# Performance work log

Hardware: AMD Instinct MI355X
Metric: run time of the kernel (lower is better)

The kernel has to match this reference:

```python
import jax, jax.numpy as jnp
from jax import lax
import numpy as np

NT, NGRID, NX = 365, 3000, 20
H, NY = 256, 1


def setup_inputs() -> dict:
    key = jax.random.key(0)
    ks = jax.random.split(key, 12)
    x = jax.random.normal(ks[0], (NT, NGRID, NX), dtype=jnp.float32)
    y = jax.random.normal(ks[1], (NT, NGRID, NY), dtype=jnp.float32)
    obs_mask = jax.random.bernoulli(ks[2], 0.7, (NT, NGRID, NY))
    y = jnp.where(obs_mask, y, jnp.nan)
    s_in = 1.0 / np.sqrt(NX + 1)
    s_h = 1.0 / np.sqrt(H)
    w_in = jax.random.uniform(ks[3], (H, NX + 1), jnp.float32, -s_in, s_in)
    b_in = jax.random.uniform(ks[4], (H,), jnp.float32, -s_in, s_in)
    w_ih = jax.random.uniform(ks[5], (4 * H, H), jnp.float32, -s_h, s_h)
    b_ih = jax.random.uniform(ks[6], (4 * H,), jnp.float32, -s_h, s_h)
    w_hh = jax.random.uniform(ks[7], (4 * H, H), jnp.float32, -s_h, s_h)
    b_hh = jax.random.uniform(ks[8], (4 * H,), jnp.float32, -s_h, s_h)
    w_out = jax.random.uniform(ks[9], (NY, H), jnp.float32, -s_h, s_h)
    b_out = jax.random.uniform(ks[10], (NY,), jnp.float32, -s_h, s_h)
    return {"x": x, "y": y, "w_in": w_in, "b_in": b_in, "w_ih": w_ih,
            "b_ih": b_ih, "w_hh": w_hh, "b_hh": b_hh, "w_out": w_out,
            "b_out": b_out}


def reference(x, y, w_in, b_in, w_ih, b_ih, w_hh, b_hh, w_out, b_out):
    nt, ngrid, nx = x.shape
    h0 = jnp.zeros((ngrid, H), x.dtype)
    c0 = jnp.zeros((ngrid, H), x.dtype)
    y0 = jnp.zeros((ngrid, NY), x.dtype)

    def step(carry, inp):
        h, c, yt = carry
        xt, yobs = inp                      # [ngrid,nx], [ngrid,ny]
        mask = ~jnp.isnan(yobs)
        yt = jnp.where(mask, yobs, yt)      # fill observed values
        xcat = jnp.concatenate([xt, yt], axis=1)          # [ngrid, nx+1]
        x0 = jax.nn.relu(xcat @ w_in.T + b_in)            # [ngrid, H]
        gates = x0 @ w_ih.T + b_ih + h @ w_hh.T + b_hh    # [ngrid, 4H]
        i, f, g, o = jnp.split(gates, 4, axis=1)
        c = jax.nn.sigmoid(f) * c + jax.nn.sigmoid(i) * jnp.tanh(g)
        h = jax.nn.sigmoid(o) * jnp.tanh(c)
        yt_new = h @ w_out.T + b_out                      # [ngrid, ny]
        return (h, c, yt_new), yt_new

    _, out = lax.scan(step, (h0, c0, y0), (x, y))
    return out  # [nt, ngrid, ny]
```

## Files before the change

kernel.cpp:

```cpp
#include <hip/hip_runtime.h>
#include <math.h>

#define NT     365
#define NGRID  3000
#define NX     20
#define H      256
#define CPB    15
#define NBLK   (NGRID/CPB)
#define THREADS 1024

#define WPK_US   (16*16*4*64*8)
#define WPKIN_US (16*2*64*8)

typedef short v8s __attribute__((ext_vector_type(8)));
typedef float v4f __attribute__((ext_vector_type(4)));
#define MFMA_BF16 __builtin_amdgcn_mfma_f32_16x16x32_bf16

__device__ __forceinline__ unsigned short f2bf(float f) {
    unsigned int u = __float_as_uint(f);
    u += 0x7fffu + ((u >> 16) & 1u);
    return (unsigned short)(u >> 16);
}
__device__ __forceinline__ float bf2f(unsigned short h) {
    return __uint_as_float(((unsigned int)h) << 16);
}
__device__ __forceinline__ float sigm(float x)  { return 1.0f / (1.0f + __expf(-x)); }
__device__ __forceinline__ float tanh_f(float x){ return 2.0f * sigm(2.0f * x) - 1.0f; }

__global__ void prep_kernel(const float* __restrict__ w_in,
                            const float* __restrict__ w_ih,
                            const float* __restrict__ w_hh,
                            const float* __restrict__ b_ih,
                            const float* __restrict__ b_hh,
                            unsigned short* __restrict__ wpk,
                            unsigned short* __restrict__ wpkin,
                            float* __restrict__ bsum) {
    int idx = blockIdx.x * 256 + threadIdx.x;
    if (idx < WPK_US) {
        int e    = idx & 7;
        int lane = (idx >> 3) & 63;
        int q    = (idx >> 9) & 3;
        int gk   = idx >> 11;
        int kap  = gk & 15, g = gk >> 4;
        int k = kap * 32 + ((lane >> 4) << 3) + e;
        int j = q * 256 + g * 16 + (lane & 15);
        float wv = (k < 256) ? w_ih[j * 256 + k] : w_hh[j * 256 + (k - 256)];
        wpk[idx] = f2bf(wv);
    }
    if (idx < WPKIN_US) {
        int e    = idx & 7;
        int lane = (idx >> 3) & 63;
        int d    = (idx >> 9) & 1;
        int tau  = idx >> 10;
        int k = ((lane >> 4) << 3) + e;
        int n = tau * 16 + (lane & 15);
        float wv = (k < NX + 1) ? w_in[n * (NX + 1) + k] : 0.0f;
        unsigned short hi = f2bf(wv);
        wpkin[idx] = d ? f2bf(wv - bf2f(hi)) : hi;
    }
    if (idx < 4 * H) bsum[idx] = b_ih[idx] + b_hh[idx];
}

__global__ __attribute__((amdgpu_flat_work_group_size(THREADS, THREADS),
                          amdgpu_waves_per_eu(4, 4)))
void lstm_main(const float* __restrict__ x,
               const float* __restrict__ y,
               const float* __restrict__ b_in,
               const float* __restrict__ w_out,
               const float* __restrict__ b_out,
               const unsigned short* __restrict__ wpk,
               const unsigned short* __restrict__ wpkin,
               const float* __restrict__ bsum,
               float* __restrict__ out) {
    __shared__ __align__(16) unsigned short Agh[16][512];
    __shared__ __align__(16) unsigned short Agl[16][512];
    __shared__ __align__(16) unsigned short Xh[512];
    __shared__ __align__(16) unsigned short Xl[512];
    __shared__ __align__(16) unsigned short Bw11[16][2048];
    __shared__ float y_part[16][16];

    const int tid  = threadIdx.x;
    const int w    = tid >> 6;
    const int lane = tid & 63;
    const int col  = lane & 15;
    const int quad = lane >> 4;
    const int g0   = blockIdx.x * CPB;

    const int   jh   = w * 16 + col;
    const float b_i  = bsum[jh];
    const float b_f  = bsum[256 + jh];
    const float b_g  = bsum[512 + jh];
    const float b_o  = bsum[768 + jh];
    const float wo   = w_out[jh];
    const float bi_x = b_in[jh];
    const float bout = b_out[0];
    const int   kq_x = jh >> 5;
    const int   kq_h = 8 + (jh >> 5);
    const int   qp_w = (jh >> 3) & 3;
    const int   e_w  = jh & 7;
    const unsigned short* bbase = wpk + (size_t)(w * 16) * 4 * 512 + lane * 8;
    const unsigned short* bx_hi = wpkin + (w * 2 + 0) * 512 + lane * 8;
    const unsigned short* bx_lo = wpkin + (w * 2 + 1) * 512 + lane * 8;

    {
        unsigned int* p;
        p = (unsigned int*)&Agh[0][0];
        for (int i = tid; i < 16 * 256; i += THREADS) p[i] = 0u;
        p = (unsigned int*)&Agl[0][0];
        for (int i = tid; i < 16 * 256; i += THREADS) p[i] = 0u;
        if (tid < 256) ((unsigned int*)&Xh[0])[tid] = 0u;
        if (tid < 256) ((unsigned int*)&Xl[0])[tid] = 0u;
    }

#define LOADK(kap, c) (*(const v8s*)(bbase + ((size_t)(kap) * 4 + (c)) * 512))
    v8s B8_0  = LOADK(8, 0),  B8_1  = LOADK(8, 1),
        B8_2  = LOADK(8, 2),  B8_3  = LOADK(8, 3);
    v8s B9_0  = LOADK(9, 0),  B9_1  = LOADK(9, 1),
        B9_2  = LOADK(9, 2),  B9_3  = LOADK(9, 3);
    v8s B10_0 = LOADK(10, 0), B10_1 = LOADK(10, 1),
        B10_2 = LOADK(10, 2), B10_3 = LOADK(10, 3);

    {
        *(v8s*)&Bw11[w][0 * 512 + lane * 8] = LOADK(11, 0);
        *(v8s*)&Bw11[w][1 * 512 + lane * 8] = LOADK(11, 1);
        *(v8s*)&Bw11[w][2 * 512 + lane * 8] = LOADK(11, 2);
        *(v8s*)&Bw11[w][3 * 512 + lane * 8] = LOADK(11, 3);
    }

    const v8s bxh = *(const v8s*)bx_hi;
    const v8s bxl = *(const v8s*)bx_lo;

    float xv = 0.0f, yv = 0.0f;
    if (tid < CPB * NX) xv = x[(size_t)g0 * NX + tid];
    if (tid < CPB)      yv = y[(size_t)g0 + tid];

    float c_st[4];
    #pragma unroll
    for (int r = 0; r < 4; ++r) c_st[r] = 0.0f;
    __syncthreads();

#define GEMM_KAP(KAP, B0, B1, B2, B3)                                   \
    {                                                                   \
        v8s Ah = *(const v8s*)&Agh[KAP][lane * 8];                      \
        v8s Al = *(const v8s*)&Agl[KAP][lane * 8];                      \
        acc0 = MFMA_BF16(Ah, B0, acc0, 0, 0, 0);                        \
        acc0 = MFMA_BF16(Al, B0, acc0, 0, 0, 0);                        \
        acc1 = MFMA_BF16(Ah, B1, acc1, 0, 0, 0);                        \
        acc1 = MFMA_BF16(Al, B1, acc1, 0, 0, 0);                        \
        acc2 = MFMA_BF16(Ah, B2, acc2, 0, 0, 0);                        \
        acc2 = MFMA_BF16(Al, B2, acc2, 0, 0, 0);                        \
        acc3 = MFMA_BF16(Ah, B3, acc3, 0, 0, 0);                        \
        acc3 = MFMA_BF16(Al, B3, acc3, 0, 0, 0);                        \
    }

    for (int t = 0; t < NT; ++t) {
        if (tid < CPB * NX) {
            float v  = xv;
            int cell = tid / NX;
            int k    = tid - cell * NX;
            int pos  = (((k >> 3) << 4) + cell) * 8 + (k & 7);
            unsigned short hi = f2bf(v);
            Xh[pos] = hi;
            Xl[pos] = f2bf(v - bf2f(hi));
        }
        if (tid < CPB) {
            if (!__builtin_isnan(yv)) {
                int pos = (2 * 16 + tid) * 8 + 4;
                unsigned short hi = f2bf(yv);
                Xh[pos] = hi;
                Xl[pos] = f2bf(yv - bf2f(hi));
            }
        }
        __syncthreads();

        {
            v8s xah = *(const v8s*)&Xh[lane * 8];
            v8s xal = *(const v8s*)&Xl[lane * 8];
            v4f xacc = {0.0f, 0.0f, 0.0f, 0.0f};
            xacc = MFMA_BF16(xah, bxh, xacc, 0, 0, 0);
            xacc = MFMA_BF16(xah, bxl, xacc, 0, 0, 0);
            xacc = MFMA_BF16(xal, bxh, xacc, 0, 0, 0);
            #pragma unroll
            for (int r = 0; r < 4; ++r) {
                int cell = quad * 4 + r;
                if (cell < CPB) {
                    float v = fmaxf(xacc[r] + bi_x, 0.0f);
                    unsigned short hi = f2bf(v);
                    int pos = (qp_w * 16 + cell) * 8 + e_w;
                    Agh[kq_x][pos] = hi;
                    Agl[kq_x][pos] = f2bf(v - bf2f(hi));
                }
            }
        }

        v4f acc0 = {0.0f, 0.0f, 0.0f, 0.0f};
        v4f acc1 = {0.0f, 0.0f, 0.0f, 0.0f};
        v4f acc2 = {0.0f, 0.0f, 0.0f, 0.0f};
        v4f acc3 = {0.0f, 0.0f, 0.0f, 0.0f};

        GEMM_KAP(8,  B8_0,  B8_1,  B8_2,  B8_3);
        GEMM_KAP(9,  B9_0,  B9_1,  B9_2,  B9_3);
        GEMM_KAP(10, B10_0, B10_1, B10_2, B10_3);

        {
            v8s Bl0 = *(const v8s*)&Bw11[w][0 * 512 + lane * 8];
            v8s Bl1 = *(const v8s*)&Bw11[w][1 * 512 + lane * 8];
            v8s Bl2 = *(const v8s*)&Bw11[w][2 * 512 + lane * 8];
            v8s Bl3 = *(const v8s*)&Bw11[w][3 * 512 + lane * 8];
            v8s Ah  = *(const v8s*)&Agh[11][lane * 8];
            v8s Al  = *(const v8s*)&Agl[11][lane * 8];
            acc0 = MFMA_BF16(Ah, Bl0, acc0, 0, 0, 0);
            acc0 = MFMA_BF16(Al, Bl0, acc0, 0, 0, 0);
            acc1 = MFMA_BF16(Ah, Bl1, acc1, 0, 0, 0);
            acc1 = MFMA_BF16(Al, Bl1, acc1, 0, 0, 0);
            acc2 = MFMA_BF16(Ah, Bl2, acc2, 0, 0, 0);
            acc2 = MFMA_BF16(Al, Bl2, acc2, 0, 0, 0);
            acc3 = MFMA_BF16(Ah, Bl3, acc3, 0, 0, 0);
            acc3 = MFMA_BF16(Al, Bl3, acc3, 0, 0, 0);
        }

        #pragma unroll 1
        for (int kap = 12; kap < 16; ++kap) {
            const unsigned short* bp = bbase + (size_t)kap * 4 * 512;
            v8s Bs0 = *(const v8s*)(bp + 0 * 512);
            v8s Bs1 = *(const v8s*)(bp + 1 * 512);
            v8s Bs2 = *(const v8s*)(bp + 2 * 512);
            v8s Bs3 = *(const v8s*)(bp + 3 * 512);
            v8s Ah  = *(const v8s*)&Agh[kap][lane * 8];
            v8s Al  = *(const v8s*)&Agl[kap][lane * 8];
            acc0 = MFMA_BF16(Ah, Bs0, acc0, 0, 0, 0);
            acc0 = MFMA_BF16(Al, Bs0, acc0, 0, 0, 0);
            acc1 = MFMA_BF16(Ah, Bs1, acc1, 0, 0, 0);
            acc1 = MFMA_BF16(Al, Bs1, acc1, 0, 0, 0);
            acc2 = MFMA_BF16(Ah, Bs2, acc2, 0, 0, 0);
            acc2 = MFMA_BF16(Al, Bs2, acc2, 0, 0, 0);
            acc3 = MFMA_BF16(Ah, Bs3, acc3, 0, 0, 0);
            acc3 = MFMA_BF16(Al, Bs3, acc3, 0, 0, 0);
        }
        __syncthreads();

        {
            const int tn = (t + 1 < NT) ? (t + 1) : t;
            if (tid < CPB * NX)
                xv = x[((size_t)tn * NGRID + g0) * NX + tid];
            if (tid < CPB)
                yv = y[(size_t)tn * NGRID + g0 + tid];
        }

        #pragma unroll 1
        for (int kap = 0; kap < 8; ++kap) {
            const unsigned short* bp = bbase + (size_t)kap * 4 * 512;
            v8s Bs0 = *(const v8s*)(bp + 0 * 512);
            v8s Bs1 = *(const v8s*)(bp + 1 * 512);
            v8s Bs2 = *(const v8s*)(bp + 2 * 512);
            v8s Bs3 = *(const v8s*)(bp + 3 * 512);
            v8s Ah  = *(const v8s*)&Agh[kap][lane * 8];
            v8s Al  = *(const v8s*)&Agl[kap][lane * 8];
            acc0 = MFMA_BF16(Ah, Bs0, acc0, 0, 0, 0);
            acc0 = MFMA_BF16(Al, Bs0, acc0, 0, 0, 0);
            acc1 = MFMA_BF16(Ah, Bs1, acc1, 0, 0, 0);
            acc1 = MFMA_BF16(Al, Bs1, acc1, 0, 0, 0);
            acc2 = MFMA_BF16(Ah, Bs2, acc2, 0, 0, 0);
            acc2 = MFMA_BF16(Al, Bs2, acc2, 0, 0, 0);
            acc3 = MFMA_BF16(Ah, Bs3, acc3, 0, 0, 0);
            acc3 = MFMA_BF16(Al, Bs3, acc3, 0, 0, 0);
        }

        {
            float yp[4];
            #pragma unroll
            for (int r = 0; r < 4; ++r) {
                int cell = quad * 4 + r;
                float iv = acc0[r] + b_i;
                float fv = acc1[r] + b_f;
                float gv = acc2[r] + b_g;
                float ov = acc3[r] + b_o;
                float c  = fmaf(sigm(fv), c_st[r], sigm(iv) * tanh_f(gv));
                c_st[r]  = c;
                float h  = sigm(ov) * tanh_f(c);
                yp[r] = 0.0f;
                if (cell < CPB) {
                    unsigned short hi = f2bf(h);
                    int pos = (qp_w * 16 + cell) * 8 + e_w;
                    Agh[kq_h][pos] = hi;
                    Agl[kq_h][pos] = f2bf(h - bf2f(hi));
                    yp[r] = h * wo;
                }
            }
            #pragma unroll
            for (int r = 0; r < 4; ++r) {
                float p = yp[r];
                p += __shfl_xor(p, 1);
                p += __shfl_xor(p, 2);
                p += __shfl_xor(p, 4);
                p += __shfl_xor(p, 8);
                if (col == 0)
                    y_part[w][quad * 4 + r] = p;
            }
        }
        __syncthreads();

        if (tid < CPB) {
            float yfin = bout;
            #pragma unroll
            for (int w2 = 0; w2 < 16; ++w2) yfin += y_part[w2][tid];
            out[(size_t)t * NGRID + g0 + tid] = yfin;
            int pos = (2 * 16 + tid) * 8 + 4;
            unsigned short hi = f2bf(yfin);
            Xh[pos] = hi;
            Xl[pos] = f2bf(yfin - bf2f(hi));
        }
    }
}

extern "C" void kernel_launch(void* const* d_in, const int* in_sizes, int n_in,
                              void* d_out, int out_size, void* d_ws, size_t ws_size,
                              hipStream_t stream) {
    const float* x     = (const float*)d_in[0];
    const float* y     = (const float*)d_in[1];
    const float* w_in  = (const float*)d_in[2];
    const float* b_in  = (const float*)d_in[3];
    const float* w_ih  = (const float*)d_in[4];
    const float* b_ih  = (const float*)d_in[5];
    const float* w_hh  = (const float*)d_in[6];
    const float* b_hh  = (const float*)d_in[7];
    const float* w_out = (const float*)d_in[8];
    const float* b_out = (const float*)d_in[9];

    unsigned short* wpk   = (unsigned short*)d_ws;
    unsigned short* wpkin = wpk + WPK_US;
    float*          bsum  = (float*)(wpkin + WPKIN_US);
    float*          out   = (float*)d_out;

    prep_kernel<<<(WPK_US + 255) / 256, 256, 0, stream>>>(
        w_in, w_ih, w_hh, b_ih, b_hh, wpk, wpkin, bsum);
    lstm_main<<<NBLK, THREADS, 0, stream>>>(
        x, y, b_in, w_out, b_out, wpk, wpkin, bsum, out);
}
```

Before: 3.968 ms.

## Double-buffer streamed weight loads across GEMM chunks and keep chunk 10 in LDS

```diff
diff --git a/kernel.cpp b/kernel.cpp
--- a/kernel.cpp
+++ b/kernel.cpp
@@ -77,6 +77,7 @@
     __shared__ __align__(16) unsigned short Xh[512];
     __shared__ __align__(16) unsigned short Xl[512];
     __shared__ __align__(16) unsigned short Bw11[16][2048];
+    __shared__ __align__(16) unsigned short Bw10[16][1536];
     __shared__ float y_part[16][16];
 
     const int tid  = threadIdx.x;
@@ -102,6 +103,14 @@
     const unsigned short* bx_hi = wpkin + (w * 2 + 0) * 512 + lane * 8;
     const unsigned short* bx_lo = wpkin + (w * 2 + 1) * 512 + lane * 8;
 
+#define BAR()                                                           \
+    do {                                                                \
+        asm volatile("s_waitcnt lgkmcnt(0)" ::: "memory");              \
+        __builtin_amdgcn_sched_barrier(0);                              \
+        __builtin_amdgcn_s_barrier();                                   \
+        __builtin_amdgcn_sched_barrier(0);                              \
+    } while (0)
+
     {
         unsigned int* p;
         p = (unsigned int*)&Agh[0][0];
@@ -113,20 +122,17 @@
     }
 
 #define LOADK(kap, c) (*(const v8s*)(bbase + ((size_t)(kap) * 4 + (c)) * 512))
-    v8s B8_0  = LOADK(8, 0),  B8_1  = LOADK(8, 1),
-        B8_2  = LOADK(8, 2),  B8_3  = LOADK(8, 3);
-    v8s B9_0  = LOADK(9, 0),  B9_1  = LOADK(9, 1),
-        B9_2  = LOADK(9, 2),  B9_3  = LOADK(9, 3);
-    v8s B10_0 = LOADK(10, 0), B10_1 = LOADK(10, 1),
-        B10_2 = LOADK(10, 2), B10_3 = LOADK(10, 3);
 
     {
         *(v8s*)&Bw11[w][0 * 512 + lane * 8] = LOADK(11, 0);
         *(v8s*)&Bw11[w][1 * 512 + lane * 8] = LOADK(11, 1);
         *(v8s*)&Bw11[w][2 * 512 + lane * 8] = LOADK(11, 2);
         *(v8s*)&Bw11[w][3 * 512 + lane * 8] = LOADK(11, 3);
-    }
-
+        *(v8s*)&Bw10[w][0 * 512 + lane * 8] = LOADK(10, 0);
+        *(v8s*)&Bw10[w][1 * 512 + lane * 8] = LOADK(10, 1);
+        *(v8s*)&Bw10[w][2 * 512 + lane * 8] = LOADK(10, 2);
+    }
+    const v8s q3b = LOADK(10, 3);
     const v8s bxh = *(const v8s*)bx_hi;
     const v8s bxl = *(const v8s*)bx_lo;
 
@@ -139,18 +145,25 @@
     for (int r = 0; r < 4; ++r) c_st[r] = 0.0f;
     __syncthreads();
 
-#define GEMM_KAP(KAP, B0, B1, B2, B3)                                   \
+    v8s sA0, sA1, sA2, sA3;
+    v8s sB0, sB1, sB2, sB3;
+
+#define ISSUE(P, KAP)                                                   \
+    P##0 = LOADK(KAP, 0); P##1 = LOADK(KAP, 1);                         \
+    P##2 = LOADK(KAP, 2); P##3 = LOADK(KAP, 3)
+
+#define GEMM_R(KAP, P)                                                  \
     {                                                                   \
         v8s Ah = *(const v8s*)&Agh[KAP][lane * 8];                      \
         v8s Al = *(const v8s*)&Agl[KAP][lane * 8];                      \
-        acc0 = MFMA_BF16(Ah, B0, acc0, 0, 0, 0);                        \
-        acc0 = MFMA_BF16(Al, B0, acc0, 0, 0, 0);                        \
-        acc1 = MFMA_BF16(Ah, B1, acc1, 0, 0, 0);                        \
-        acc1 = MFMA_BF16(Al, B1, acc1, 0, 0, 0);                        \
-        acc2 = MFMA_BF16(Ah, B2, acc2, 0, 0, 0);                        \
-        acc2 = MFMA_BF16(Al, B2, acc2, 0, 0, 0);                        \
-        acc3 = MFMA_BF16(Ah, B3, acc3, 0, 0, 0);                        \
-        acc3 = MFMA_BF16(Al, B3, acc3, 0, 0, 0);                        \
+        acc0 = MFMA_BF16(Ah, P##0, acc0, 0, 0, 0);                      \
+        acc0 = MFMA_BF16(Al, P##0, acc0, 0, 0, 0);                      \
+        acc1 = MFMA_BF16(Ah, P##1, acc1, 0, 0, 0);                      \
+        acc1 = MFMA_BF16(Al, P##1, acc1, 0, 0, 0);                      \
+        acc2 = MFMA_BF16(Ah, P##2, acc2, 0, 0, 0);                      \
+        acc2 = MFMA_BF16(Al, P##2, acc2, 0, 0, 0);                      \
+        acc3 = MFMA_BF16(Ah, P##3, acc3, 0, 0, 0);                      \
+        acc3 = MFMA_BF16(Al, P##3, acc3, 0, 0, 0);                      \
     }
 
     for (int t = 0; t < NT; ++t) {
@@ -171,7 +184,9 @@
                 Xl[pos] = f2bf(yv - bf2f(hi));
             }
         }
-        __syncthreads();
+        ISSUE(sA, 8);
+        BAR();
+        ISSUE(sB, 9);
 
         {
             v8s xah = *(const v8s*)&Xh[lane * 8];
@@ -198,10 +213,28 @@
         v4f acc2 = {0.0f, 0.0f, 0.0f, 0.0f};
         v4f acc3 = {0.0f, 0.0f, 0.0f, 0.0f};
 
-        GEMM_KAP(8,  B8_0,  B8_1,  B8_2,  B8_3);
-        GEMM_KAP(9,  B9_0,  B9_1,  B9_2,  B9_3);
-        GEMM_KAP(10, B10_0, B10_1, B10_2, B10_3);
-
+        GEMM_R(8, sA);   ISSUE(sA, 12);
+        GEMM_R(9, sB);   ISSUE(sB, 13);
+        GEMM_R(12, sA);  ISSUE(sA, 14);
+        GEMM_R(13, sB);  ISSUE(sB, 15);
+        GEMM_R(14, sA);  ISSUE(sA, 0);
+        GEMM_R(15, sB);
+
+        {
+            v8s Bl0 = *(const v8s*)&Bw10[w][0 * 512 + lane * 8];
+            v8s Bl1 = *(const v8s*)&Bw10[w][1 * 512 + lane * 8];
+            v8s Bl2 = *(const v8s*)&Bw10[w][2 * 512 + lane * 8];
+            v8s Ah  = *(const v8s*)&Agh[10][lane * 8];
+            v8s Al  = *(const v8s*)&Agl[10][lane * 8];
+            acc0 = MFMA_BF16(Ah, Bl0, acc0, 0, 0, 0);
+            acc0 = MFMA_BF16(Al, Bl0, acc0, 0, 0, 0);
+            acc1 = MFMA_BF16(Ah, Bl1, acc1, 0, 0, 0);
+            acc1 = MFMA_BF16(Al, Bl1, acc1, 0, 0, 0);
+            acc2 = MFMA_BF16(Ah, Bl2, acc2, 0, 0, 0);
+            acc2 = MFMA_BF16(Al, Bl2, acc2, 0, 0, 0);
+            acc3 = MFMA_BF16(Ah, q3b, acc3, 0, 0, 0);
+            acc3 = MFMA_BF16(Al, q3b, acc3, 0, 0, 0);
+        }
         {
             v8s Bl0 = *(const v8s*)&Bw11[w][0 * 512 + lane * 8];
             v8s Bl1 = *(const v8s*)&Bw11[w][1 * 512 + lane * 8];
@@ -218,26 +251,7 @@
             acc3 = MFMA_BF16(Ah, Bl3, acc3, 0, 0, 0);
             acc3 = MFMA_BF16(Al, Bl3, acc3, 0, 0, 0);
         }
-
-        #pragma unroll 1
-        for (int kap = 12; kap < 16; ++kap) {
-            const unsigned short* bp = bbase + (size_t)kap * 4 * 512;
-            v8s Bs0 = *(const v8s*)(bp + 0 * 512);
-            v8s Bs1 = *(const v8s*)(bp + 1 * 512);
-            v8s Bs2 = *(const v8s*)(bp + 2 * 512);
-            v8s Bs3 = *(const v8s*)(bp + 3 * 512);
-            v8s Ah  = *(const v8s*)&Agh[kap][lane * 8];
-            v8s Al  = *(const v8s*)&Agl[kap][lane * 8];
-            acc0 = MFMA_BF16(Ah, Bs0, acc0, 0, 0, 0);
-            acc0 = MFMA_BF16(Al, Bs0, acc0, 0, 0, 0);
-            acc1 = MFMA_BF16(Ah, Bs1, acc1, 0, 0, 0);
-            acc1 = MFMA_BF16(Al, Bs1, acc1, 0, 0, 0);
-            acc2 = MFMA_BF16(Ah, Bs2, acc2, 0, 0, 0);
-            acc2 = MFMA_BF16(Al, Bs2, acc2, 0, 0, 0);
-            acc3 = MFMA_BF16(Ah, Bs3, acc3, 0, 0, 0);
-            acc3 = MFMA_BF16(Al, Bs3, acc3, 0, 0, 0);
-        }
-        __syncthreads();
+        BAR();
 
         {
             const int tn = (t + 1 < NT) ? (t + 1) : t;
@@ -247,24 +261,14 @@
                 yv = y[(size_t)tn * NGRID + g0 + tid];
         }
 
-        #pragma unroll 1
-        for (int kap = 0; kap < 8; ++kap) {
-            const unsigned short* bp = bbase + (size_t)kap * 4 * 512;
-            v8s Bs0 = *(const v8s*)(bp + 0 * 512);
-            v8s Bs1 = *(const v8s*)(bp + 1 * 512);
-            v8s Bs2 = *(const v8s*)(bp + 2 * 512);
-            v8s Bs3 = *(const v8s*)(bp + 3 * 512);
-            v8s Ah  = *(const v8s*)&Agh[kap][lane * 8];
-            v8s Al  = *(const v8s*)&Agl[kap][lane * 8];
-            acc0 = MFMA_BF16(Ah, Bs0, acc0, 0, 0, 0);
-            acc0 = MFMA_BF16(Al, Bs0, acc0, 0, 0, 0);
-            acc1 = MFMA_BF16(Ah, Bs1, acc1, 0, 0, 0);
-            acc1 = MFMA_BF16(Al, Bs1, acc1, 0, 0, 0);
-            acc2 = MFMA_BF16(Ah, Bs2, acc2, 0, 0, 0);
-            acc2 = MFMA_BF16(Al, Bs2, acc2, 0, 0, 0);
-            acc3 = MFMA_BF16(Ah, Bs3, acc3, 0, 0, 0);
-            acc3 = MFMA_BF16(Al, Bs3, acc3, 0, 0, 0);
-        }
+        GEMM_R(0, sA);   ISSUE(sB, 1);
+        GEMM_R(1, sB);   ISSUE(sA, 2);
+        GEMM_R(2, sA);   ISSUE(sB, 3);
+        GEMM_R(3, sB);   ISSUE(sA, 4);
+        GEMM_R(4, sA);   ISSUE(sB, 5);
+        GEMM_R(5, sB);   ISSUE(sA, 6);
+        GEMM_R(6, sA);   ISSUE(sB, 7);
+        GEMM_R(7, sB);
 
         {
             float yp[4];
@@ -298,7 +302,7 @@
                     y_part[w][quad * 4 + r] = p;
             }
         }
-        __syncthreads();
+        BAR();
 
         if (tid < CPB) {
             float yfin = bout;
```

New measurement: 8.552 ms. +115.5%, slower.
